# Kernel tuning notes

Measured on AMD Instinct MI355X. Metric: run time of the kernel, lower is better.

## Reference

```python
import jax, jax.numpy as jnp
import numpy as np

B, I, C, D_IN, D_OUT = 256, 2048, 10, 8, 16
ROUTING_ITERS = 3


def squash(s, eps=1e-9):
    # s: [..., d]; magnitude squashed to (0, 1)
    sq = jnp.sum(s * s, axis=-1, keepdims=True)
    return (sq / (1.0 + sq)) * s / jnp.sqrt(sq + eps)


def setup_inputs() -> dict:
    key = jax.random.key(0)
    k_u, k_w = jax.random.split(key)
    u = jax.random.normal(k_u, (B, I, D_IN), dtype=jnp.float32)
    # torch lazy-init: W ~ randn([1, I, C, D_OUT, D_IN]); leading 1 dropped (broadcast).
    W = jax.random.normal(k_w, (I, C, D_OUT, D_IN), dtype=jnp.float32)
    return {"u": u, "W": W}


def reference(u, W):
    # u_hat[b,i,c,o] = sum_d W[i,c,o,d] * u[b,i,d]  (broadcast instead of W.repeat)
    u_hat = jnp.einsum('icod,bid->bico', W, u)  # [B, I, C, D_OUT]
    b_ij = jnp.zeros(u_hat.shape[:3] + (1,), dtype=u_hat.dtype)  # [B, I, C, 1]
    v_j = None
    for it in range(ROUTING_ITERS):
        c_ij = jax.nn.softmax(b_ij, axis=2)                 # over output capsules
        s_j = jnp.sum(c_ij * u_hat, axis=1, keepdims=True)   # [B, 1, C, D_OUT]
        v_j = squash(s_j)
        if it < ROUTING_ITERS - 1:
            a_ij = jnp.sum(u_hat * v_j, axis=-1, keepdims=True)  # agreement
            b_ij = b_ij + a_ij
    return v_j.squeeze(1)  # [B, C, D_OUT]
```

## Files before the change

kernel.cpp:

```cpp
#include <hip/hip_runtime.h>
#include <math.h>

#define BB 256
#define II 2048
#define CC 10
#define DOUT 16
#define COW 160
#define WELEMS (II*CC*DOUT*8)
#define BT 16
#define LEN 64
#define IW 16
#define NSPLIT (II/LEN)

typedef short  short8v __attribute__((ext_vector_type(8)));
typedef float  f32x4   __attribute__((ext_vector_type(4)));

__device__ __forceinline__ ushort f2bf(float x) {
    union { float f; unsigned u; } v; v.f = x;
    unsigned r = v.u + 0x7fff + ((v.u >> 16) & 1);
    return (ushort)(r >> 16);
}
__device__ __forceinline__ float bf2f(ushort h) {
    union { unsigned u; float f; } v; v.u = ((unsigned)h) << 16; return v.f;
}
__device__ __forceinline__ short8v pack8(float a0, float a1, float a2, float a3,
                                         float b0, float b1, float b2, float b3) {
    short8v r;
    r[0]=(short)f2bf(a0); r[1]=(short)f2bf(a1); r[2]=(short)f2bf(a2); r[3]=(short)f2bf(a3);
    r[4]=(short)f2bf(b0); r[5]=(short)f2bf(b1); r[6]=(short)f2bf(b2); r[7]=(short)f2bf(b3);
    return r;
}

__global__ __launch_bounds__(256)
void wcvt(const float* __restrict__ W, ushort* __restrict__ Wb)
{
    const size_t e = ((size_t)blockIdx.x * 256 + threadIdx.x) * 8;
    const float4 x0 = *(const float4*)(W + e);
    const float4 x1 = *(const float4*)(W + e + 4);
    *(short8v*)(Wb + e) = pack8(x0.x, x0.y, x0.z, x0.w, x1.x, x1.y, x1.z, x1.w);
}

template<int MODE>
__global__ __launch_bounds__(256, 3)
void caps_route(const float* __restrict__ u, const ushort* __restrict__ Wb,
                const float* __restrict__ v0, const float* __restrict__ v1,
                float* __restrict__ p)
{
    __shared__ union {
        ushort us[BT * LEN * 8];
        float  red[4 * CC * 4 * BT * 4];
    } sm;

    const int tid = threadIdx.x;
    const int l   = tid & 63;
    const int w   = tid >> 6;
    const int bl  = l & 15;
    const int g   = l >> 4;
    const int bbase = blockIdx.y * BT;
    const int b_abs = bbase + bl;
    const int i0    = blockIdx.x * LEN;

    for (int e = tid; e < BT * LEN * 2; e += 256) {
        const int rb = e / (LEN * 2), rem = e % (LEN * 2);
        const int i = rem >> 1, dh = (rem & 1) * 4;
        const float4 x = *(const float4*)(u + ((size_t)(bbase + rb) * II + i0 + i) * 8 + dh);
        ushort4 h;
        h.x = f2bf(x.x); h.y = f2bf(x.y); h.z = f2bf(x.z); h.w = f2bf(x.w);
        *(ushort4*)&sm.us[(rb * LEN + (i ^ (rb & 7))) * 8 + dh] = h;
    }

    float vreg[CC][4];
    if constexpr (MODE >= 1) {
#pragma unroll
        for (int c = 0; c < CC; ++c) {
            float4 x = *(const float4*)(v0 + b_abs * COW + c * DOUT + 4 * g);
            if constexpr (MODE == 2) {
                const float4 y = *(const float4*)(v1 + b_abs * COW + c * DOUT + 4 * g);
                x.x += y.x; x.y += y.y; x.z += y.z; x.w += y.w;
            }
            vreg[c][0] = x.x; vreg[c][1] = x.y; vreg[c][2] = x.z; vreg[c][3] = x.w;
        }
    }

    f32x4 acc[CC];
#pragma unroll
    for (int c = 0; c < CC; ++c) acc[c] = (f32x4){0.f, 0.f, 0.f, 0.f};
    const short8v zero8 = {0,0,0,0,0,0,0,0};
    const f32x4   zacc  = (f32x4){0.f, 0.f, 0.f, 0.f};

    __syncthreads();

#pragma unroll
    for (int iq = 0; iq < IW / 4; ++iq) {
        const int ig   = i0 + w * IW + iq * 4;
        const int iloc = w * IW + iq * 4;
        const short8v u8 = *(const short8v*)
            &sm.us[(bl * LEN + ((iloc + g) ^ (bl & 7))) * 8];

        if constexpr (MODE == 0) {
#pragma unroll
            for (int c = 0; c < CC; ++c) {
                const short8v w8 = *(const short8v*)
                    &Wb[((size_t)(ig + g) * CC + c) * 128 + bl * 8];
                acc[c] = __builtin_amdgcn_mfma_f32_16x16x32_bf16(w8, u8, acc[c], 0, 0, 0);
            }
        } else {
            float uf[8];
#pragma unroll
            for (int e = 0; e < 8; ++e) uf[e] = bf2f((ushort)u8[e]);

            float tk[CC];
#pragma unroll
            for (int c = 0; c < CC; ++c) {
                const short8v w8 = *(const short8v*)
                    &Wb[((size_t)(ig + g) * CC + c) * 128 + bl * 8];
                f32x4 uh[4];
#pragma unroll
                for (int j = 0; j < 4; ++j)
                    uh[j] = __builtin_amdgcn_mfma_f32_16x16x32_bf16(
                        w8, (g == j) ? u8 : zero8, zacc, 0, 0, 0);
                float d0 = uh[0][0]*vreg[c][0] + uh[0][1]*vreg[c][1]
                         + uh[0][2]*vreg[c][2] + uh[0][3]*vreg[c][3];
                float d1 = uh[1][0]*vreg[c][0] + uh[1][1]*vreg[c][1]
                         + uh[1][2]*vreg[c][2] + uh[1][3]*vreg[c][3];
                float d2 = uh[2][0]*vreg[c][0] + uh[2][1]*vreg[c][1]
                         + uh[2][2]*vreg[c][2] + uh[2][3]*vreg[c][3];
                float d3 = uh[3][0]*vreg[c][0] + uh[3][1]*vreg[c][1]
                         + uh[3][2]*vreg[c][2] + uh[3][3]*vreg[c][3];
                d0 += __shfl_xor(d0, 16); d0 += __shfl_xor(d0, 32);
                d1 += __shfl_xor(d1, 16); d1 += __shfl_xor(d1, 32);
                d2 += __shfl_xor(d2, 16); d2 += __shfl_xor(d2, 32);
                d3 += __shfl_xor(d3, 16); d3 += __shfl_xor(d3, 32);
                float sel = d0;
                sel = (g == 1) ? d1 : sel;
                sel = (g == 2) ? d2 : sel;
                sel = (g == 3) ? d3 : sel;
                tk[c] = sel;
            }

            float s = 0.f;
#pragma unroll
            for (int c = 0; c < CC; ++c) { tk[c] = __expf(tk[c]); s += tk[c]; }
            const float inv = 1.f / s;

#pragma unroll
            for (int c = 0; c < CC; ++c) {
                const float cw = tk[c] * inv;
                const short8v w8 = *(const short8v*)
                    &Wb[((size_t)(ig + g) * CC + c) * 128 + bl * 8];
                const short8v bfB = pack8(cw*uf[0], cw*uf[1], cw*uf[2], cw*uf[3],
                                          cw*uf[4], cw*uf[5], cw*uf[6], cw*uf[7]);
                acc[c] = __builtin_amdgcn_mfma_f32_16x16x32_bf16(w8, bfB, acc[c], 0, 0, 0);
            }
        }
    }

    __syncthreads();
#pragma unroll
    for (int c = 0; c < CC; ++c)
        *(f32x4*)&sm.red[(((w * CC + c) * 4 + g) * BT + bl) * 4] = acc[c];
    __syncthreads();

    float* pp = p + (size_t)blockIdx.x * (BB * COW) + (size_t)b_abs * COW;
    for (int c = w * 3; c < CC && c < w * 3 + 3; ++c) {
        f32x4 sacc = (f32x4){0.f, 0.f, 0.f, 0.f};
#pragma unroll
        for (int ww = 0; ww < 4; ++ww) {
            const f32x4 t = *(const f32x4*)&sm.red[(((ww * CC + c) * 4 + g) * BT + bl) * 4];
            sacc[0] += t[0]; sacc[1] += t[1]; sacc[2] += t[2]; sacc[3] += t[3];
        }
        *(float4*)(pp + c * DOUT + 4 * g) =
            make_float4(sacc[0], sacc[1], sacc[2], sacc[3]);
    }
}

__global__ __launch_bounds__(64)
void reduce_squash(const float* __restrict__ p, int nsplit, float scale,
                   float* __restrict__ vout)
{
    const int bc = blockIdx.x;
    const int b = bc / CC, c = bc % CC;
    const int l = threadIdx.x;
    const int o = l & 15, g = l >> 4;
    const float* base = p + (size_t)b * COW + c * DOUT + o;

    float s0 = 0.f, s1 = 0.f;
    for (int sp = g; sp < nsplit; sp += 8)
        s0 += base[(size_t)sp * (BB * COW)];
    for (int sp = g + 4; sp < nsplit; sp += 8)
        s1 += base[(size_t)sp * (BB * COW)];
    float s = s0 + s1;
    s += __shfl_xor(s, 16);
    s += __shfl_xor(s, 32);
    s *= scale;
    float sq = s * s;
    sq += __shfl_xor(sq, 1);
    sq += __shfl_xor(sq, 2);
    sq += __shfl_xor(sq, 4);
    sq += __shfl_xor(sq, 8);
    const float sc = (sq / (1.f + sq)) * rsqrtf(sq + 1e-9f);
    if (l < 16) vout[b * COW + c * DOUT + o] = s * sc;
}

extern "C" void kernel_launch(void* const* d_in, const int* in_sizes, int n_in,
                              void* d_out, int out_size, void* d_ws, size_t ws_size,
                              hipStream_t stream)
{
    const float* u = (const float*)d_in[0];
    const float* W = (const float*)d_in[1];
    float* out = (float*)d_out;

    const size_t SEG = (size_t)BB * COW;
    float*  v0 = (float*)d_ws;
    float*  v1 = v0 + SEG;
    ushort* Wb = (ushort*)(v1 + SEG);
    float*  p  = (float*)(Wb + WELEMS);

    dim3 grid(NSPLIT, BB / BT);

    wcvt<<<WELEMS / (256 * 8), 256, 0, stream>>>(W, Wb);
    caps_route<0><<<grid, 256, 0, stream>>>(u, Wb, nullptr, nullptr, p);
    reduce_squash<<<BB * CC, 64, 0, stream>>>(p, NSPLIT, 0.1f, v0);
    caps_route<1><<<grid, 256, 0, stream>>>(u, Wb, v0, v0, p);
    reduce_squash<<<BB * CC, 64, 0, stream>>>(p, NSPLIT, 1.f, v1);
    caps_route<2><<<grid, 256, 0, stream>>>(u, Wb, v0, v1, p);
    reduce_squash<<<BB * CC, 64, 0, stream>>>(p, NSPLIT, 1.f, out);
}
```

Measured before the change: 93.83 us.

## Fuse W bf16 conversion into first routing pass and precompute v0+v1 sum

Drops the separate W conversion kernel. The first routing pass now reads fp32 W directly, converts it in registers, and the blockIdx.y==0 blocks write the bf16 copy for the later passes. reduce_squash also writes v0+v1 into a new buffer, so the third pass can reuse MODE 1 with a single v input instead of loading two. This removes one launch and the standalone W read/write pass. In exchange, the first pass's MFMA loop reads W at double the width and converts every element in every block, and it also switches f2bf to the library intrinsic.

```diff
diff --git a/kernel.cpp b/kernel.cpp
--- a/kernel.cpp
+++ b/kernel.cpp
@@ -1,4 +1,5 @@
 #include <hip/hip_runtime.h>
+#include <hip/hip_bf16.h>
 #include <math.h>
 
 #define BB 256
@@ -16,9 +17,7 @@
 typedef float  f32x4   __attribute__((ext_vector_type(4)));
 
 __device__ __forceinline__ ushort f2bf(float x) {
-    union { float f; unsigned u; } v; v.f = x;
-    unsigned r = v.u + 0x7fff + ((v.u >> 16) & 1);
-    return (ushort)(r >> 16);
+    return __bfloat16_as_ushort(__float2bfloat16(x));
 }
 __device__ __forceinline__ float bf2f(ushort h) {
     union { unsigned u; float f; } v; v.u = ((unsigned)h) << 16; return v.f;
@@ -31,19 +30,10 @@
     return r;
 }
 
-__global__ __launch_bounds__(256)
-void wcvt(const float* __restrict__ W, ushort* __restrict__ Wb)
-{
-    const size_t e = ((size_t)blockIdx.x * 256 + threadIdx.x) * 8;
-    const float4 x0 = *(const float4*)(W + e);
-    const float4 x1 = *(const float4*)(W + e + 4);
-    *(short8v*)(Wb + e) = pack8(x0.x, x0.y, x0.z, x0.w, x1.x, x1.y, x1.z, x1.w);
-}
-
 template<int MODE>
 __global__ __launch_bounds__(256, 3)
-void caps_route(const float* __restrict__ u, const ushort* __restrict__ Wb,
-                const float* __restrict__ v0, const float* __restrict__ v1,
+void caps_route(const float* __restrict__ u, const float* __restrict__ Wf,
+                ushort* __restrict__ Wb, const float* __restrict__ vv,
                 float* __restrict__ p)
 {
     __shared__ union {
@@ -60,6 +50,15 @@
     const int b_abs = bbase + bl;
     const int i0    = blockIdx.x * LEN;
 
+    float vreg[CC][4];
+    if constexpr (MODE >= 1) {
+#pragma unroll
+        for (int c = 0; c < CC; ++c) {
+            const float4 x = *(const float4*)(vv + b_abs * COW + c * DOUT + 4 * g);
+            vreg[c][0] = x.x; vreg[c][1] = x.y; vreg[c][2] = x.z; vreg[c][3] = x.w;
+        }
+    }
+
     for (int e = tid; e < BT * LEN * 2; e += 256) {
         const int rb = e / (LEN * 2), rem = e % (LEN * 2);
         const int i = rem >> 1, dh = (rem & 1) * 4;
@@ -69,19 +68,6 @@
         *(ushort4*)&sm.us[(rb * LEN + (i ^ (rb & 7))) * 8 + dh] = h;
     }
 
-    float vreg[CC][4];
-    if constexpr (MODE >= 1) {
-#pragma unroll
-        for (int c = 0; c < CC; ++c) {
-            float4 x = *(const float4*)(v0 + b_abs * COW + c * DOUT + 4 * g);
-            if constexpr (MODE == 2) {
-                const float4 y = *(const float4*)(v1 + b_abs * COW + c * DOUT + 4 * g);
-                x.x += y.x; x.y += y.y; x.z += y.z; x.w += y.w;
-            }
-            vreg[c][0] = x.x; vreg[c][1] = x.y; vreg[c][2] = x.z; vreg[c][3] = x.w;
-        }
-    }
-
     f32x4 acc[CC];
 #pragma unroll
     for (int c = 0; c < CC; ++c) acc[c] = (f32x4){0.f, 0.f, 0.f, 0.f};
@@ -100,8 +86,12 @@
         if constexpr (MODE == 0) {
 #pragma unroll
             for (int c = 0; c < CC; ++c) {
-                const short8v w8 = *(const short8v*)
-                    &Wb[((size_t)(ig + g) * CC + c) * 128 + bl * 8];
+                const size_t widx = ((size_t)(ig + g) * CC + c) * 128 + bl * 8;
+                const float4 w0 = *(const float4*)(Wf + widx);
+                const float4 w1 = *(const float4*)(Wf + widx + 4);
+                const short8v w8 = pack8(w0.x, w0.y, w0.z, w0.w,
+                                         w1.x, w1.y, w1.z, w1.w);
+                if (blockIdx.y == 0) *(short8v*)&Wb[widx] = w8;
                 acc[c] = __builtin_amdgcn_mfma_f32_16x16x32_bf16(w8, u8, acc[c], 0, 0, 0);
             }
         } else {
@@ -176,7 +166,8 @@
 
 __global__ __launch_bounds__(64)
 void reduce_squash(const float* __restrict__ p, int nsplit, float scale,
-                   float* __restrict__ vout)
+                   float* __restrict__ vout, const float* __restrict__ vprev,
+                   float* __restrict__ vsout)
 {
     const int bc = blockIdx.x;
     const int b = bc / CC, c = bc % CC;
@@ -199,7 +190,12 @@
     sq += __shfl_xor(sq, 4);
     sq += __shfl_xor(sq, 8);
     const float sc = (sq / (1.f + sq)) * rsqrtf(sq + 1e-9f);
-    if (l < 16) vout[b * COW + c * DOUT + o] = s * sc;
+    if (l < 16) {
+        const int idx = b * COW + c * DOUT + o;
+        const float v = s * sc;
+        vout[idx] = v;
+        if (vsout) vsout[idx] = v + vprev[idx];
+    }
 }
 
 extern "C" void kernel_launch(void* const* d_in, const int* in_sizes, int n_in,
@@ -213,16 +209,16 @@
     const size_t SEG = (size_t)BB * COW;
     float*  v0 = (float*)d_ws;
     float*  v1 = v0 + SEG;
-    ushort* Wb = (ushort*)(v1 + SEG);
+    float*  vs = v1 + SEG;
+    ushort* Wb = (ushort*)(vs + SEG);
     float*  p  = (float*)(Wb + WELEMS);
 
     dim3 grid(NSPLIT, BB / BT);
 
-    wcvt<<<WELEMS / (256 * 8), 256, 0, stream>>>(W, Wb);
-    caps_route<0><<<grid, 256, 0, stream>>>(u, Wb, nullptr, nullptr, p);
-    reduce_squash<<<BB * CC, 64, 0, stream>>>(p, NSPLIT, 0.1f, v0);
-    caps_route<1><<<grid, 256, 0, stream>>>(u, Wb, v0, v0, p);
-    reduce_squash<<<BB * CC, 64, 0, stream>>>(p, NSPLIT, 1.f, v1);
-    caps_route<2><<<grid, 256, 0, stream>>>(u, Wb, v0, v1, p);
-    reduce_squash<<<BB * CC, 64, 0, stream>>>(p, NSPLIT, 1.f, out);
-}
+    caps_route<0><<<grid, 256, 0, stream>>>(u, W, Wb, nullptr, p);
+    reduce_squash<<<BB * CC, 64, 0, stream>>>(p, NSPLIT, 0.1f, v0, nullptr, nullptr);
+    caps_route<1><<<grid, 256, 0, stream>>>(u, nullptr, Wb, v0, p);
+    reduce_squash<<<BB * CC, 64, 0, stream>>>(p, NSPLIT, 1.f, v1, v0, vs);
+    caps_route<1><<<grid, 256, 0, stream>>>(u, nullptr, Wb, vs, p);
+    reduce_squash<<<BB * CC, 64, 0, stream>>>(p, NSPLIT, 1.f, out, nullptr, nullptr);
+}
```

Result: slower. 110.8 us (+18.1%).
